# Kernel tuning notes

Hardware: AMD Instinct MI355X
Metric: run time of the kernel (lower is better)

Reference implementation:

```python
import jax, jax.numpy as jnp
import numpy as np

N = 100000
E = 1600000
IN_DIM = 128
HID = 64
EPS = 1e-5


def setup_inputs() -> dict:
    key = jax.random.key(0)
    ks = jax.random.split(key, 16)
    x = jax.random.normal(ks[0], (N, IN_DIM), dtype=jnp.float32)
    edge_index = jax.random.randint(ks[1], (2, E), 0, N, dtype=jnp.int32)
    def glorot(k, fan_in, fan_out):
        s = jnp.sqrt(6.0 / (fan_in + fan_out))
        return jax.random.uniform(k, (fan_in, fan_out), jnp.float32, -s, s)
    return {
        "x": x,
        "edge_index": edge_index,
        "W0": glorot(ks[2], IN_DIM, HID), "b0": jnp.zeros((HID,), jnp.float32),
        "W1": glorot(ks[3], HID, HID),    "b1": jnp.zeros((HID,), jnp.float32),
        "W2": glorot(ks[4], HID, HID),    "b2": jnp.zeros((HID,), jnp.float32),
        "g0": jnp.ones((HID,), jnp.float32),  "be0": jnp.zeros((HID,), jnp.float32),
        "g1": jnp.ones((HID,), jnp.float32),  "be1": jnp.zeros((HID,), jnp.float32),
        "g2": jnp.ones((HID,), jnp.float32),  "be2": jnp.zeros((HID,), jnp.float32),
        "fc1_w": glorot(ks[5], HID, 32), "fc1_b": jnp.zeros((32,), jnp.float32),
        "fc2_w": glorot(ks[6], 32, 2),   "fc2_b": jnp.zeros((2,), jnp.float32),
    }


def _gcn_conv(x, src, dst, dis, W, b):
    # x' = D^{-1/2} (A + I) D^{-1/2} (x W) + b ; dis = deg^{-1/2} with self-loops
    h = x @ W                                   # [N, H]
    norm = dis[src] * dis[dst]                  # [E]
    msg = h[src] * norm[:, None]                # [E, H]
    agg = jax.ops.segment_sum(msg, dst, num_segments=N)
    agg = agg + h * (dis * dis)[:, None]        # self-loop contribution
    return agg + b


def _batchnorm(x, gamma, beta):
    mu = jnp.mean(x, axis=0)
    var = jnp.mean(jnp.square(x - mu), axis=0)  # biased, as torch BN training
    return gamma * (x - mu) * jax.lax.rsqrt(var + EPS) + beta


def reference(x, edge_index, W0, b0, W1, b1, W2, b2,
              g0, be0, g1, be1, g2, be2, fc1_w, fc1_b, fc2_w, fc2_b):
    src = edge_index[0]
    dst = edge_index[1]
    deg = jax.ops.segment_sum(jnp.ones((E,), x.dtype), dst, num_segments=N) + 1.0
    dis = jax.lax.rsqrt(deg)                    # deg >= 1 from self-loops
    for W, b, g, be in ((W0, b0, g0, be0), (W1, b1, g1, be1), (W2, b2, g2, be2)):
        x = _gcn_conv(x, src, dst, dis, W, b)
        x = jax.nn.relu(_batchnorm(x, g, be))
        # dropout: identity (deterministic eval)
    x = jax.nn.relu(x @ fc1_w + fc1_b)
    x = x @ fc2_w + fc2_b
    return jax.nn.log_softmax(x, axis=1)
```

## Files before the change

### kernel.cpp

```cpp
#include <hip/hip_runtime.h>
#include <hip/hip_fp16.h>
#include <math.h>


#define BUCK_CAP 6144
#define PB_EDGES 8192
#define GATH_BLOCKS 2048

typedef _Float16 f16x8 __attribute__((ext_vector_type(8)));
typedef float f32x4 __attribute__((ext_vector_type(4)));

union H4U { uint2 u; __half h[4]; };
union H8U { uint4 u; __half h[8]; };

__device__ inline uint2 pack4(float a, float b, float c, float d) {
    H4U t;
    t.h[0] = __float2half_rn(a); t.h[1] = __float2half_rn(b);
    t.h[2] = __float2half_rn(c); t.h[3] = __float2half_rn(d);
    return t.u;
}
__device__ inline float4 unpack4(uint2 u) {
    H4U t; t.u = u;
    return make_float4(__half2float(t.h[0]), __half2float(t.h[1]),
                       __half2float(t.h[2]), __half2float(t.h[3]));
}
__device__ inline void upadd8(uint4 u, float* a) {
    H8U t; t.u = u;
#pragma unroll
    for (int i = 0; i < 8; ++i) a[i] += __half2float(t.h[i]);
}

__global__ __launch_bounds__(256) void k_zero(int* __restrict__ gcur,
                                              float* __restrict__ stats) {
    int t = threadIdx.x;
    gcur[t] = 0; gcur[t + 256] = 0;
#pragma unroll
    for (int k = 0; k < 12; ++k) stats[k * 256 + t] = 0.f;
}

__global__ __launch_bounds__(256) void k_part(const int* __restrict__ src,
                                              const int* __restrict__ dst,
                                              int* __restrict__ gcur,
                                              unsigned* __restrict__ rec,
                                              int E, int NB) {
    __shared__ int hist[512];
    __shared__ int lbase[512];
    __shared__ int gbase[512];
    __shared__ int stmp[256];
    __shared__ unsigned stage[PB_EDGES];
    __shared__ unsigned short sbkt[PB_EDGES];
    const int tid = threadIdx.x;
    const int e0 = blockIdx.x * PB_EDGES;
    const int e1 = min(e0 + PB_EDGES, E);
    const int cnt = e1 - e0;

    hist[tid] = 0; hist[tid + 256] = 0;
    __syncthreads();
    for (int i = e0 + tid; i < e1; i += 256)
        atomicAdd(&hist[dst[i] >> 8], 1);
    __syncthreads();
    for (int b = tid; b < NB; b += 256) {
        int c = hist[b];
        gbase[b] = c ? atomicAdd(&gcur[b], c) : 0;
    }
    int h0 = hist[2 * tid], h1 = hist[2 * tid + 1];
    int psum = h0 + h1;
    stmp[tid] = psum;
    __syncthreads();
    int x = psum;
    for (int off = 1; off < 256; off <<= 1) {
        int y = (tid >= off) ? stmp[tid - off] : 0;
        __syncthreads();
        x += y;
        stmp[tid] = x;
        __syncthreads();
    }
    int excl = x - psum;
    lbase[2 * tid] = excl;
    lbase[2 * tid + 1] = excl + h0;
    __syncthreads();
    hist[2 * tid] = excl;
    hist[2 * tid + 1] = excl + h0;
    __syncthreads();
    for (int i = e0 + tid; i < e1; i += 256) {
        int s = src[i], d = dst[i];
        int b = d >> 8;
        int pos = atomicAdd(&hist[b], 1);
        stage[pos] = ((unsigned)s << 8) | (unsigned)(d & 255);
        sbkt[pos] = (unsigned short)b;
    }
    __syncthreads();
    for (int i = tid; i < cnt; i += 256) {
        int b = sbkt[i];
        rec[(size_t)b * BUCK_CAP + gbase[b] + (i - lbase[b])] = stage[i];
    }
}

__global__ __launch_bounds__(256) void k_bscat(const int* __restrict__ gcur,
                                               const unsigned* __restrict__ rec,
                                               float* __restrict__ dis,
                                               int* __restrict__ row_ptr,
                                               int* __restrict__ ssrc,
                                               int n, int NB, int E) {
    __shared__ int h[256];
    __shared__ int cur[256];
    __shared__ int lb[512];
    __shared__ int stmp[256];
    __shared__ int stage[BUCK_CAP];
    const int b = blockIdx.x, tid = threadIdx.x;
    int g0 = (2 * tid < NB) ? gcur[2 * tid] : 0;
    int g1 = (2 * tid + 1 < NB) ? gcur[2 * tid + 1] : 0;
    int ps = g0 + g1;
    stmp[tid] = ps;
    h[tid] = 0;
    __syncthreads();
    int xx = ps;
    for (int off = 1; off < 256; off <<= 1) {
        int y = (tid >= off) ? stmp[tid - off] : 0;
        __syncthreads();
        xx += y;
        stmp[tid] = xx;
        __syncthreads();
    }
    int ex = xx - ps;
    lb[2 * tid] = ex;
    lb[2 * tid + 1] = ex + g0;
    __syncthreads();
    const int bb = lb[b];
    if (b == 0 && tid == 0) row_ptr[n] = E;

    const int cnt = gcur[b];
    const unsigned* r = rec + (size_t)b * BUCK_CAP;
    for (int i = tid; i < cnt; i += 256)
        atomicAdd(&h[r[i] & 255u], 1);
    __syncthreads();
    const int myd = h[tid];
    const int node = b * 256 + tid;
    if (node < n) dis[node] = rsqrtf((float)myd + 1.0f);
    int x = myd;
    for (int off = 1; off < 256; off <<= 1) {
        int y = (tid >= off) ? h[tid - off] : 0;
        __syncthreads();
        x += y;
        h[tid] = x;
        __syncthreads();
    }
    const int excl = x - myd;
    if (node < n) row_ptr[node] = bb + excl;
    cur[tid] = excl;
    __syncthreads();
    for (int i = tid; i < cnt; i += 256) {
        unsigned v = r[i];
        int pos = atomicAdd(&cur[v & 255u], 1);
        stage[pos] = (int)(v >> 8);
    }
    __syncthreads();
    for (int i = tid; i < cnt; i += 256) ssrc[bb + i] = stage[i];
}

template <int K, bool BN, bool XH>
__global__ __launch_bounds__(256) void k_gemm(const void* __restrict__ Xv,
                                              const float* __restrict__ W,
                                              const float* __restrict__ dis,
                                              const float* __restrict__ stats,
                                              const float* __restrict__ g,
                                              const float* __restrict__ be,
                                              __half* __restrict__ Hp, int n) {
    constexpr int KS = K / 32;
    constexpr int XSTR = K + 8;
    __shared__ __align__(16) __half BF[KS * 4 * 64 * 8];
    __shared__ __align__(16) __half XL[64 * XSTR];
    __shared__ float muS[64], wS[64], bS[64];
    const int tid = threadIdx.x;
    const int row0 = blockIdx.x * 64;

    if constexpr (BN) {
        if (tid < 64) {
            float s1 = 0.f, s2 = 0.f;
#pragma unroll
            for (int r = 0; r < 8; ++r) {
                s1 += stats[r * 128 + tid];
                s2 += stats[r * 128 + 64 + tid];
            }
            float inv_n = 1.0f / (float)n;
            float m = s1 * inv_n;
            float var = s2 * inv_n - m * m;
            muS[tid] = m;
            wS[tid] = rsqrtf(var + 1e-5f) * g[tid];
            bS[tid] = be[tid];
        }
    }
    for (int i = tid; i < KS * 4 * 64; i += 256) {
        int l = i & 63, fs = i >> 6;
        int ks = fs >> 2, ct = fs & 3;
        int kb = ks * 32 + ((l >> 4) << 3);
        int c = (ct << 4) + (l & 15);
        H8U t;
#pragma unroll
        for (int j = 0; j < 8; ++j) t.h[j] = __float2half_rn(W[(kb + j) * 64 + c]);
        *reinterpret_cast<uint4*>(&BF[i * 8]) = t.u;
    }
    __syncthreads();

    if constexpr (!XH) {
        constexpr int Q4 = K / 4;
        const float4* X4 = (const float4*)Xv;
        for (int it = 0; it < 64 * Q4 / 256; ++it) {
            int idx = it * 256 + tid;
            int row = idx / Q4, q = idx % Q4;
            int grow = row0 + row;
            float4 v = make_float4(0.f, 0.f, 0.f, 0.f);
            if (grow < n) v = X4[(size_t)grow * Q4 + q];
            *reinterpret_cast<uint2*>(&XL[row * XSTR + q * 4]) = pack4(v.x, v.y, v.z, v.w);
        }
    } else {
        constexpr int QU = K / 4;
        const uint2* Xh = (const uint2*)Xv;
        for (int it = 0; it < 64 * QU / 256; ++it) {
            int idx = it * 256 + tid;
            int row = idx / QU, q = idx % QU;
            int grow = row0 + row;
            float4 v = make_float4(0.f, 0.f, 0.f, 0.f);
            if (grow < n) {
                v = unpack4(Xh[(size_t)grow * QU + q]);
                float4 m = *reinterpret_cast<const float4*>(&muS[q * 4]);
                float4 w4 = *reinterpret_cast<const float4*>(&wS[q * 4]);
                float4 b4 = *reinterpret_cast<const float4*>(&bS[q * 4]);
                v.x = fmaxf((v.x - m.x) * w4.x + b4.x, 0.f);
                v.y = fmaxf((v.y - m.y) * w4.y + b4.y, 0.f);
                v.z = fmaxf((v.z - m.z) * w4.z + b4.z, 0.f);
                v.w = fmaxf((v.w - m.w) * w4.w + b4.w, 0.f);
            }
            *reinterpret_cast<uint2*>(&XL[row * XSTR + q * 4]) = pack4(v.x, v.y, v.z, v.w);
        }
    }
    __syncthreads();

    const int wave = tid >> 6, lane = tid & 63;
    const __half* arow = &XL[(wave * 16 + (lane & 15)) * XSTR + ((lane >> 4) << 3)];
    f16x8 a[KS];
#pragma unroll
    for (int ks = 0; ks < KS; ++ks)
        a[ks] = *reinterpret_cast<const f16x8*>(arow + ks * 32);

    f32x4 acc[4];
#pragma unroll
    for (int ct = 0; ct < 4; ++ct) acc[ct] = (f32x4){0.f, 0.f, 0.f, 0.f};
#pragma unroll
    for (int ct = 0; ct < 4; ++ct)
#pragma unroll
        for (int ks = 0; ks < KS; ++ks) {
            f16x8 b = *reinterpret_cast<const f16x8*>(&BF[((ks * 4 + ct) * 64 + lane) * 8]);
            acc[ct] = __builtin_amdgcn_mfma_f32_16x16x32_f16(a[ks], b, acc[ct], 0, 0, 0);
        }

    const int mbase = row0 + wave * 16 + ((lane >> 4) << 2);
#pragma unroll
    for (int reg = 0; reg < 4; ++reg) {
        int grow = mbase + reg;
        if (grow < n) {
            float dd = dis[grow];
#pragma unroll
            for (int ct = 0; ct < 4; ++ct)
                Hp[(size_t)grow * 64 + ct * 16 + (lane & 15)] =
                    __float2half_rn(acc[ct][reg] * dd);
        }
    }
}

__global__ __launch_bounds__(256) void k_gather(const int* __restrict__ row_ptr,
                                                const int* __restrict__ ssrc,
                                                const float* __restrict__ dis,
                                                const uint4* __restrict__ Hp,
                                                uint4* __restrict__ AGG,
                                                float* __restrict__ stats, int n) {
    __shared__ float red[32][64];
    const int tid = threadIdx.x;
    const int g = tid >> 3, fi = tid & 7;
    float sacc[8] = {}, qacc[8] = {};
    for (int d = blockIdx.x * 32 + g; d < n; d += gridDim.x * 32) {
        int r0 = row_ptr[d], r1 = row_ptr[d + 1];
        float a[8] = {};
        upadd8(Hp[(size_t)d * 8 + fi], a);
        int p = r0;
        for (; p + 7 < r1; p += 8) {
            int s0 = ssrc[p], s1 = ssrc[p + 1], s2 = ssrc[p + 2], s3 = ssrc[p + 3];
            int s4 = ssrc[p + 4], s5 = ssrc[p + 5], s6 = ssrc[p + 6], s7 = ssrc[p + 7];
            uint4 q0 = Hp[(size_t)s0 * 8 + fi];
            uint4 q1 = Hp[(size_t)s1 * 8 + fi];
            uint4 q2 = Hp[(size_t)s2 * 8 + fi];
            uint4 q3 = Hp[(size_t)s3 * 8 + fi];
            uint4 q4 = Hp[(size_t)s4 * 8 + fi];
            uint4 q5 = Hp[(size_t)s5 * 8 + fi];
            uint4 q6 = Hp[(size_t)s6 * 8 + fi];
            uint4 q7 = Hp[(size_t)s7 * 8 + fi];
            upadd8(q0, a); upadd8(q1, a); upadd8(q2, a); upadd8(q3, a);
            upadd8(q4, a); upadd8(q5, a); upadd8(q6, a); upadd8(q7, a);
        }
        for (; p + 3 < r1; p += 4) {
            int s0 = ssrc[p], s1 = ssrc[p + 1], s2 = ssrc[p + 2], s3 = ssrc[p + 3];
            uint4 q0 = Hp[(size_t)s0 * 8 + fi];
            uint4 q1 = Hp[(size_t)s1 * 8 + fi];
            uint4 q2 = Hp[(size_t)s2 * 8 + fi];
            uint4 q3 = Hp[(size_t)s3 * 8 + fi];
            upadd8(q0, a); upadd8(q1, a); upadd8(q2, a); upadd8(q3, a);
        }
        for (; p < r1; ++p) upadd8(Hp[(size_t)ssrc[p] * 8 + fi], a);
        float dd = dis[d];
        H8U o;
#pragma unroll
        for (int i = 0; i < 8; ++i) {
            float v = a[i] * dd;
            o.h[i] = __float2half_rn(v);
            sacc[i] += v;
            qacc[i] += v * v;
        }
        AGG[(size_t)d * 8 + fi] = o.u;
    }
#pragma unroll
    for (int j = 0; j < 8; ++j) red[g][fi * 8 + j] = sacc[j];
    __syncthreads();
    if (tid < 64) {
        float s = 0.f;
#pragma unroll
        for (int r = 0; r < 32; ++r) s += red[r][tid];
        atomicAdd(&stats[(blockIdx.x & 7) * 128 + tid], s);
    }
    __syncthreads();
#pragma unroll
    for (int j = 0; j < 8; ++j) red[g][fi * 8 + j] = qacc[j];
    __syncthreads();
    if (tid < 64) {
        float s = 0.f;
#pragma unroll
        for (int r = 0; r < 32; ++r) s += red[r][tid];
        atomicAdd(&stats[(blockIdx.x & 7) * 128 + 64 + tid], s);
    }
}

__global__ __launch_bounds__(256) void k_head(const uint2* __restrict__ X,
                                              const float* __restrict__ stats,
                                              const float* __restrict__ g,
                                              const float* __restrict__ be,
                                              const float* __restrict__ w1,
                                              const float* __restrict__ b1,
                                              const float* __restrict__ w2,
                                              const float* __restrict__ b2,
                                              float* __restrict__ out, int n) {
    __shared__ __align__(16) float w1s[64 * 32];
    __shared__ __align__(16) float b1s[32];
    __shared__ float w2s[64];
    __shared__ float b2s[2];
    __shared__ float muS[64], wS[64], bS[64];
    int tid = threadIdx.x;
    for (int i = tid; i < 512; i += 256)
        reinterpret_cast<float4*>(w1s)[i] = reinterpret_cast<const float4*>(w1)[i];
    if (tid < 32) b1s[tid] = b1[tid];
    if (tid >= 64 && tid < 128) w2s[tid - 64] = w2[tid - 64];
    if (tid >= 128 && tid < 130) b2s[tid - 128] = b2[tid - 128];
    if (tid < 64) {
        float s1 = 0.f, s2 = 0.f;
#pragma unroll
        for (int r = 0; r < 8; ++r) {
            s1 += stats[r * 128 + tid];
            s2 += stats[r * 128 + 64 + tid];
        }
        float inv_n = 1.0f / (float)n;
        float m = s1 * inv_n;
        float var = s2 * inv_n - m * m;
        muS[tid] = m;
        wS[tid] = rsqrtf(var + 1e-5f) * g[tid];
        bS[tid] = be[tid];
    }
    __syncthreads();
    int row = blockIdx.x * 256 + tid;
    if (row >= n) return;

    float4 h[8];
#pragma unroll
    for (int j4 = 0; j4 < 8; ++j4) h[j4] = reinterpret_cast<float4*>(b1s)[j4];

#pragma unroll
    for (int k4 = 0; k4 < 16; ++k4) {
        float4 xv = unpack4(X[(size_t)row * 16 + k4]);
#pragma unroll
        for (int kk = 0; kk < 4; ++kk) {
            int k = k4 * 4 + kk;
            float raw = (kk == 0) ? xv.x : (kk == 1) ? xv.y : (kk == 2) ? xv.z : xv.w;
            float xk = fmaxf((raw - muS[k]) * wS[k] + bS[k], 0.f);
            const float4* wrow = reinterpret_cast<const float4*>(&w1s[k * 32]);
#pragma unroll
            for (int j4 = 0; j4 < 8; ++j4) {
                float4 wv = wrow[j4];
                h[j4].x += xk * wv.x; h[j4].y += xk * wv.y;
                h[j4].z += xk * wv.z; h[j4].w += xk * wv.w;
            }
        }
    }
    float o0 = b2s[0], o1 = b2s[1];
#pragma unroll
    for (int j4 = 0; j4 < 8; ++j4) {
        float hv[4] = {h[j4].x, h[j4].y, h[j4].z, h[j4].w};
#pragma unroll
        for (int c = 0; c < 4; ++c) {
            float hj = fmaxf(hv[c], 0.f);
            int j = j4 * 4 + c;
            o0 += hj * w2s[2 * j];
            o1 += hj * w2s[2 * j + 1];
        }
    }
    float m = fmaxf(o0, o1);
    float l = __logf(__expf(o0 - m) + __expf(o1 - m));
    reinterpret_cast<float2*>(out)[row] = make_float2(o0 - m - l, o1 - m - l);
}

extern "C" void kernel_launch(void* const* d_in, const int* in_sizes, int n_in,
                              void* d_out, int out_size, void* d_ws, size_t ws_size,
                              hipStream_t stream) {
    const float* x    = (const float*)d_in[0];
    const int*   ei   = (const int*)d_in[1];
    const float* W0   = (const float*)d_in[2];
    const float* W1   = (const float*)d_in[4];
    const float* W2   = (const float*)d_in[6];
    const float* g0   = (const float*)d_in[8];
    const float* be0  = (const float*)d_in[9];
    const float* g1   = (const float*)d_in[10];
    const float* be1  = (const float*)d_in[11];
    const float* g2   = (const float*)d_in[12];
    const float* be2  = (const float*)d_in[13];
    const float* fc1w = (const float*)d_in[14];
    const float* fc1b = (const float*)d_in[15];
    const float* fc2w = (const float*)d_in[16];
    const float* fc2b = (const float*)d_in[17];

    const int N = in_sizes[0] / 128;
    const int E = in_sizes[1] / 2;
    const int* srcp = ei;
    const int* dstp = ei + E;
    const int NB = (N + 255) >> 8;

    char* ws = (char*)d_ws;
    size_t off = 0;
    auto alloc = [&](size_t bytes) -> void* {
        void* p = ws + off;
        off = (off + bytes + 255) & ~(size_t)255;
        return p;
    };
    int*      gcur    = (int*)alloc(512 * 4);
    float*    stats   = (float*)alloc(3 * 8 * 128 * 4);
    float*    dis     = (float*)alloc((size_t)N * 4);
    int*      row_ptr = (int*)alloc((size_t)(N + 1) * 4);
    unsigned* rec     = (unsigned*)alloc((size_t)NB * BUCK_CAP * 4);
    int*      ssrc    = (int*)alloc((size_t)E * 4);
    __half*   B0      = (__half*)alloc((size_t)N * 64 * 2);
    __half*   B1      = (__half*)alloc((size_t)N * 64 * 2);

    k_zero<<<1, 256, 0, stream>>>(gcur, stats);
    k_part<<<(E + PB_EDGES - 1) / PB_EDGES, 256, 0, stream>>>(srcp, dstp, gcur, rec, E, NB);
    k_bscat<<<NB, 256, 0, stream>>>(gcur, rec, dis, row_ptr, ssrc, N, NB, E);

    const int gemm_grid = (N + 63) / 64;

    k_gemm<128, false, false><<<gemm_grid, 256, 0, stream>>>(x, W0, dis, nullptr, nullptr, nullptr, B0, N);
    k_gather<<<GATH_BLOCKS, 256, 0, stream>>>(row_ptr, ssrc, dis, (const uint4*)B0, (uint4*)B1, stats + 0, N);

    k_gemm<64, true, true><<<gemm_grid, 256, 0, stream>>>(B1, W1, dis, stats + 0, g0, be0, B0, N);
    k_gather<<<GATH_BLOCKS, 256, 0, stream>>>(row_ptr, ssrc, dis, (const uint4*)B0, (uint4*)B1, stats + 1024, N);

    k_gemm<64, true, true><<<gemm_grid, 256, 0, stream>>>(B1, W2, dis, stats + 1024, g1, be1, B0, N);
    k_gather<<<GATH_BLOCKS, 256, 0, stream>>>(row_ptr, ssrc, dis, (const uint4*)B0, (uint4*)B1, stats + 2048, N);

    k_head<<<(N + 255) / 256, 256, 0, stream>>>((const uint2*)B1, stats + 2048, g2, be2,
                                                fc1w, fc1b, fc2w, fc2b,
                                                (float*)d_out, N);
}
```

Before: 218.9 us.

## Drop shared-memory staging in edge partition and bucket scatter kernels

```diff
diff --git a/kernel.cpp b/kernel.cpp
--- a/kernel.cpp
+++ b/kernel.cpp
@@ -5,7 +5,6 @@
 
 #define BUCK_CAP 6144
 #define PB_EDGES 8192
-#define GATH_BLOCKS 2048
 
 typedef _Float16 f16x8 __attribute__((ext_vector_type(8)));
 typedef float f32x4 __attribute__((ext_vector_type(4)));
@@ -38,61 +37,47 @@
     for (int k = 0; k < 12; ++k) stats[k * 256 + t] = 0.f;
 }
 
-__global__ __launch_bounds__(256) void k_part(const int* __restrict__ src,
+__global__ __launch_bounds__(512) void k_part(const int* __restrict__ src,
                                               const int* __restrict__ dst,
                                               int* __restrict__ gcur,
                                               unsigned* __restrict__ rec,
                                               int E, int NB) {
     __shared__ int hist[512];
-    __shared__ int lbase[512];
     __shared__ int gbase[512];
-    __shared__ int stmp[256];
-    __shared__ unsigned stage[PB_EDGES];
-    __shared__ unsigned short sbkt[PB_EDGES];
     const int tid = threadIdx.x;
     const int e0 = blockIdx.x * PB_EDGES;
     const int e1 = min(e0 + PB_EDGES, E);
-    const int cnt = e1 - e0;
-
-    hist[tid] = 0; hist[tid + 256] = 0;
-    __syncthreads();
-    for (int i = e0 + tid; i < e1; i += 256)
-        atomicAdd(&hist[dst[i] >> 8], 1);
-    __syncthreads();
-    for (int b = tid; b < NB; b += 256) {
-        int c = hist[b];
-        gbase[b] = c ? atomicAdd(&gcur[b], c) : 0;
-    }
-    int h0 = hist[2 * tid], h1 = hist[2 * tid + 1];
-    int psum = h0 + h1;
-    stmp[tid] = psum;
-    __syncthreads();
-    int x = psum;
-    for (int off = 1; off < 256; off <<= 1) {
-        int y = (tid >= off) ? stmp[tid - off] : 0;
-        __syncthreads();
-        x += y;
-        stmp[tid] = x;
-        __syncthreads();
-    }
-    int excl = x - psum;
-    lbase[2 * tid] = excl;
-    lbase[2 * tid + 1] = excl + h0;
-    __syncthreads();
-    hist[2 * tid] = excl;
-    hist[2 * tid + 1] = excl + h0;
-    __syncthreads();
-    for (int i = e0 + tid; i < e1; i += 256) {
-        int s = src[i], d = dst[i];
-        int b = d >> 8;
-        int pos = atomicAdd(&hist[b], 1);
-        stage[pos] = ((unsigned)s << 8) | (unsigned)(d & 255);
-        sbkt[pos] = (unsigned short)b;
-    }
-    __syncthreads();
-    for (int i = tid; i < cnt; i += 256) {
-        int b = sbkt[i];
-        rec[(size_t)b * BUCK_CAP + gbase[b] + (i - lbase[b])] = stage[i];
+    hist[tid] = 0;
+    __syncthreads();
+    int dloc[PB_EDGES / 512];
+#pragma unroll
+    for (int it = 0; it < PB_EDGES / 512; ++it) {
+        int i = e0 + it * 512 + tid;
+        if (i < e1) {
+            int d = dst[i];
+            dloc[it] = d;
+            atomicAdd(&hist[d >> 8], 1);
+        } else dloc[it] = -1;
+    }
+    __syncthreads();
+    if (tid < NB) {
+        int c = hist[tid];
+        gbase[tid] = c ? atomicAdd(&gcur[tid], c) : 0;
+    }
+    __syncthreads();
+    hist[tid] = 0;
+    __syncthreads();
+#pragma unroll
+    for (int it = 0; it < PB_EDGES / 512; ++it) {
+        int d = dloc[it];
+        if (d >= 0) {
+            int i = e0 + it * 512 + tid;
+            int b = d >> 8;
+            int s = src[i];
+            int off = atomicAdd(&hist[b], 1);
+            rec[(size_t)b * BUCK_CAP + gbase[b] + off] =
+                ((unsigned)s << 8) | (unsigned)(d & 255);
+        }
     }
 }
 
@@ -106,7 +91,6 @@
     __shared__ int cur[256];
     __shared__ int lb[512];
     __shared__ int stmp[256];
-    __shared__ int stage[BUCK_CAP];
     const int b = blockIdx.x, tid = threadIdx.x;
     int g0 = (2 * tid < NB) ? gcur[2 * tid] : 0;
     int g1 = (2 * tid + 1 < NB) ? gcur[2 * tid + 1] : 0;
@@ -147,15 +131,13 @@
     }
     const int excl = x - myd;
     if (node < n) row_ptr[node] = bb + excl;
-    cur[tid] = excl;
+    cur[tid] = bb + excl;
     __syncthreads();
     for (int i = tid; i < cnt; i += 256) {
         unsigned v = r[i];
         int pos = atomicAdd(&cur[v & 255u], 1);
-        stage[pos] = (int)(v >> 8);
-    }
-    __syncthreads();
-    for (int i = tid; i < cnt; i += 256) ssrc[bb + i] = stage[i];
+        ssrc[pos] = (int)(v >> 8);
+    }
 }
 
 template <int K, bool BN, bool XH>
@@ -456,19 +438,19 @@
     __half*   B1      = (__half*)alloc((size_t)N * 64 * 2);
 
     k_zero<<<1, 256, 0, stream>>>(gcur, stats);
-    k_part<<<(E + PB_EDGES - 1) / PB_EDGES, 256, 0, stream>>>(srcp, dstp, gcur, rec, E, NB);
+    k_part<<<(E + PB_EDGES - 1) / PB_EDGES, 512, 0, stream>>>(srcp, dstp, gcur, rec, E, NB);
     k_bscat<<<NB, 256, 0, stream>>>(gcur, rec, dis, row_ptr, ssrc, N, NB, E);
 
     const int gemm_grid = (N + 63) / 64;
 
     k_gemm<128, false, false><<<gemm_grid, 256, 0, stream>>>(x, W0, dis, nullptr, nullptr, nullptr, B0, N);
-    k_gather<<<GATH_BLOCKS, 256, 0, stream>>>(row_ptr, ssrc, dis, (const uint4*)B0, (uint4*)B1, stats + 0, N);
+    k_gather<<<2048, 256, 0, stream>>>(row_ptr, ssrc, dis, (const uint4*)B0, (uint4*)B1, stats + 0, N);
 
     k_gemm<64, true, true><<<gemm_grid, 256, 0, stream>>>(B1, W1, dis, stats + 0, g0, be0, B0, N);
-    k_gather<<<GATH_BLOCKS, 256, 0, stream>>>(row_ptr, ssrc, dis, (const uint4*)B0, (uint4*)B1, stats + 1024, N);
+    k_gather<<<2048, 256, 0, stream>>>(row_ptr, ssrc, dis, (const uint4*)B0, (uint4*)B1, stats + 1024, N);
 
     k_gemm<64, true, true><<<gemm_grid, 256, 0, stream>>>(B1, W2, dis, stats + 1024, g1, be1, B0, N);
-    k_gather<<<GATH_BLOCKS, 256, 0, stream>>>(row_ptr, ssrc, dis, (const uint4*)B0, (uint4*)B1, stats + 2048, N);
+    k_gather<<<2048, 256, 0, stream>>>(row_ptr, ssrc, dis, (const uint4*)B0, (uint4*)B1, stats + 2048, N);
 
     k_head<<<(N + 255) / 256, 256, 0, stream>>>((const uint2*)B1, stats + 2048, g2, be2,
                                                 fc1w, fc1b, fc2w, fc2b,
```

New measurement: 217.2 us. No clear change (-0.8%).
